# Kernel tuning notes

Hardware: AMD Instinct MI355X
Metric: run time of the kernel (lower is better)

Reference implementation:

```python
import jax, jax.numpy as jnp
import numpy as np

L, H, D, A, T = 2, 8, 512, 64, 256  # layers, heads, model_dim, attention_dim, target_dim
B, S = 2, 2048
EPS = 1e-5


def _ln(x, g, b):
    m = jnp.mean(x, axis=-1, keepdims=True)
    v = jnp.mean((x - m) ** 2, axis=-1, keepdims=True)
    return (x - m) / jnp.sqrt(v + EPS) * g + b


def setup_inputs() -> dict:
    key = jax.random.key(0)
    ks = jax.random.split(key, 16)
    s = 0.02
    inp = {
        "x": jax.random.normal(ks[0], (B, S, D), jnp.float32),
        # per-head QKV projections, stacked over layers and heads
        "Wq": jax.random.normal(ks[1], (L, H, D, A), jnp.float32) * s,
        "bq": jnp.zeros((L, H, A), jnp.float32),
        "Wk": jax.random.normal(ks[2], (L, H, D, A), jnp.float32) * s,
        "bk": jnp.zeros((L, H, A), jnp.float32),
        "Wv": jax.random.normal(ks[3], (L, H, D, A), jnp.float32) * s,
        "bv": jnp.zeros((L, H, A), jnp.float32),
        # output projection of concatenated heads: [H*A, D]
        "Wo": jax.random.normal(ks[4], (L, H * A, D), jnp.float32) * s,
        "bo": jnp.zeros((L, D), jnp.float32),
        # AddNorm after attention
        "ln1_g": jnp.ones((L, D), jnp.float32),
        "ln1_b": jnp.zeros((L, D), jnp.float32),
        # FFN (hidden_dim == model_dim in this module)
        "W1": jax.random.normal(ks[5], (L, D, D), jnp.float32) * s,
        "b1": jnp.zeros((L, D), jnp.float32),
        "W2": jax.random.normal(ks[6], (L, D, D), jnp.float32) * s,
        "b2": jnp.zeros((L, D), jnp.float32),
        # AddNorm after FFN
        "ln2_g": jnp.ones((L, D), jnp.float32),
        "ln2_b": jnp.zeros((L, D), jnp.float32),
        # final projection to target_dim
        "Wp": jax.random.normal(ks[7], (D, T), jnp.float32) * s,
        "bp": jnp.zeros((T,), jnp.float32),
    }
    return inp


def reference(x, Wq, bq, Wk, bk, Wv, bv, Wo, bo, ln1_g, ln1_b,
              W1, b1, W2, b2, ln2_g, ln2_b, Wp, bp):
    scale = 1.0 / jnp.sqrt(jnp.asarray(A, x.dtype))
    for i in range(L):
        # batched per-head QKV projections (math identical to per-head Linears)
        q = jnp.einsum('bsd,hda->bhsa', x, Wq[i]) + bq[i][:, None, :]
        k = jnp.einsum('bsd,hda->bhsa', x, Wk[i]) + bk[i][:, None, :]
        v = jnp.einsum('bsd,hda->bhsa', x, Wv[i]) + bv[i][:, None, :]
        scores = jnp.einsum('bhsa,bhta->bhst', q, k) * scale  # [B,H,S,S]
        attn = jax.nn.softmax(scores, axis=-1)
        heads = jnp.einsum('bhst,bhta->bhsa', attn, v)        # [B,H,S,A]
        concat = heads.transpose(0, 2, 1, 3).reshape(x.shape[0], x.shape[1], H * A)
        mha = concat @ Wo[i] + bo[i]
        x = _ln(x + mha, ln1_g[i], ln1_b[i])
        ffn = jax.nn.relu(x @ W1[i] + b1[i]) @ W2[i] + b2[i]
        x = _ln(x + ffn, ln2_g[i], ln2_b[i])
    return x @ Wp + bp
```

## Files before the change

kernel.cpp:

```cpp
#include <hip/hip_runtime.h>
#include <hip/hip_bf16.h>

#define MDIM 4096
#define DDIM 512
#define ADIM 64
#define HHEADS 8
#define SLEN 2048
#define TDIM 256

typedef __attribute__((ext_vector_type(8))) short short8;
typedef __attribute__((ext_vector_type(16))) float f32x16;

__device__ __forceinline__ unsigned short f2bf(float f) {
    union { __hip_bfloat16 h; unsigned short u; } c;
    c.h = __float2bfloat16(f);
    return c.u;
}
__device__ __forceinline__ float bf2f(short s) {
    return __uint_as_float((unsigned)(unsigned short)s << 16);
}

#define N1 524288
#define N2 524288
#define NP 131072
__global__ __launch_bounds__(256) void prep_k(
    const float* __restrict__ Wq, const float* __restrict__ Wk, const float* __restrict__ Wv,
    const float* __restrict__ Wo, const float* __restrict__ W1, const float* __restrict__ W2,
    const float* __restrict__ Wp, const float* __restrict__ x,
    short* __restrict__ Wqt, short* __restrict__ Wkt, short* __restrict__ Wvt,
    short* __restrict__ Wot, short* __restrict__ W1t, short* __restrict__ W2t,
    short* __restrict__ Wpt, short* __restrict__ xbf)
{
    long idx = (long)blockIdx.x * 256 + threadIdx.x;
    if (idx < 3L * N1) {
        int t = (int)(idx / N1);
        int r = (int)(idx % N1);
        int a = r & 63, k = (r >> 6) & 511, hh = r >> 15;
        const float* src = (t == 0) ? Wq : (t == 1) ? Wk : Wv;
        short* dst = (t == 0) ? Wqt : (t == 1) ? Wkt : Wvt;
        dst[((size_t)hh << 15) + (a << 9) + k] = (short)f2bf(src[r]);
        return;
    }
    idx -= 3L * N1;
    if (idx < 3L * N2) {
        int t = (int)(idx / N2);
        int r = (int)(idx % N2);
        int n = r & 511, k = (r >> 9) & 511, i = r >> 18;
        const float* src = (t == 0) ? Wo : (t == 1) ? W1 : W2;
        short* dst = (t == 0) ? Wot : (t == 1) ? W1t : W2t;
        dst[((size_t)i << 18) + (n << 9) + k] = (short)f2bf(src[r]);
        return;
    }
    idx -= 3L * N2;
    if (idx < NP) {
        int r = (int)idx;
        int n = r & 255, k = r >> 8;
        Wpt[n * 512 + k] = (short)f2bf(Wp[r]);
        return;
    }
    idx -= NP;
    xbf[idx] = (short)f2bf(x[idx]);
}

#define LDT 66
__global__ __launch_bounds__(256, 2) void gemm_bf(
    const short* __restrict__ A, const short* __restrict__ Bt,
    const float* __restrict__ bias, void* __restrict__ Cout,
    int M, int N, int K, int flags)
{
    __shared__ short As[64 * LDT];
    __shared__ short Bs[64 * LDT];
    const int tid = threadIdx.x;
    const int wave = tid >> 6, lane = tid & 63;
    const int l31 = lane & 31, hi = lane >> 5;
    const int wm = wave >> 1, wn = wave & 1;
    const int m0 = blockIdx.y * 64, n0 = blockIdx.x * 64;

    f32x16 acc;
#pragma unroll
    for (int r = 0; r < 16; ++r) acc[r] = 0.f;

    const int sr = tid >> 2;
    const int sc = (tid & 3) * 16;

    for (int k0 = 0; k0 < K; k0 += 64) {
        __syncthreads();
        *(short8*)&As[sr * LDT + sc]     = *(const short8*)&A[(size_t)(m0 + sr) * K + k0 + sc];
        *(short8*)&As[sr * LDT + sc + 8] = *(const short8*)&A[(size_t)(m0 + sr) * K + k0 + sc + 8];
        *(short8*)&Bs[sr * LDT + sc]     = *(const short8*)&Bt[(size_t)(n0 + sr) * K + k0 + sc];
        *(short8*)&Bs[sr * LDT + sc + 8] = *(const short8*)&Bt[(size_t)(n0 + sr) * K + k0 + sc + 8];
        __syncthreads();

        short8 af[4], bfm[4];
#pragma unroll
        for (int ks = 0; ks < 4; ++ks) {
            af[ks]  = *(const short8*)&As[(wm * 32 + l31) * LDT + ks * 16 + hi * 8];
            bfm[ks] = *(const short8*)&Bs[(wn * 32 + l31) * LDT + ks * 16 + hi * 8];
        }
#pragma unroll
        for (int ks = 0; ks < 4; ++ks)
            acc = __builtin_amdgcn_mfma_f32_32x32x16_bf16(af[ks], bfm[ks], acc, 0, 0, 0);
    }

    const int col = n0 + wn * 32 + l31;
    const float bb = bias[col];
    const int rbase = m0 + wm * 32 + 4 * hi;
#pragma unroll
    for (int r = 0; r < 16; ++r) {
        int row = rbase + (r & 3) + 8 * (r >> 2);
        float v = acc[r] + bb;
        if (flags & 1) v = fmaxf(v, 0.f);
        if (flags & 2) ((short*)Cout)[(size_t)row * N + col] = (short)f2bf(v);
        else           ((float*)Cout)[(size_t)row * N + col] = v;
    }
}

#define EXPC 0.1803368801111244f

__global__ __launch_bounds__(256, 2) void qkv_bf(
    const short* __restrict__ A,
    const short* __restrict__ Wqt, const short* __restrict__ Wkt, const short* __restrict__ Wvt,
    const float* __restrict__ bq, const float* __restrict__ bk, const float* __restrict__ bv,
    short* __restrict__ Oq, short* __restrict__ Ok, short* __restrict__ Ov)
{
    __shared__ short As[128 * LDT];
    __shared__ short Bs[64 * LDT];
    const int tid = threadIdx.x;
    const int wave = tid >> 6, lane = tid & 63;
    const int l31 = lane & 31, hi = lane >> 5;
    const int wm = wave >> 1, wn = wave & 1;
    const int m0 = blockIdx.y * 128;
    const int nt = blockIdx.x;
    const int which = nt >> 3, h = nt & 7;

    const short* Bt = ((which == 0) ? Wqt : (which == 1) ? Wkt : Wvt) + (size_t)h * 64 * 512;
    const float* bias = ((which == 0) ? bq : (which == 1) ? bk : bv) + h * 64;
    short* Out = (which == 0) ? Oq : (which == 1) ? Ok : Ov;

    f32x16 acc[2];
#pragma unroll
    for (int ms = 0; ms < 2; ++ms)
#pragma unroll
        for (int r = 0; r < 16; ++r) acc[ms][r] = 0.f;

    const int sr = tid >> 3;
    const int sc = (tid & 7) * 8;

    for (int k0 = 0; k0 < 512; k0 += 64) {
        __syncthreads();
#pragma unroll
        for (int p = 0; p < 4; ++p)
            *(short8*)&As[(p * 32 + sr) * LDT + sc] =
                *(const short8*)&A[(size_t)(m0 + p * 32 + sr) * 512 + k0 + sc];
#pragma unroll
        for (int p = 0; p < 2; ++p)
            *(short8*)&Bs[(p * 32 + sr) * LDT + sc] =
                *(const short8*)&Bt[(size_t)(p * 32 + sr) * 512 + k0 + sc];
        __syncthreads();

        short8 af[2][4], bfm[4];
#pragma unroll
        for (int ms = 0; ms < 2; ++ms)
#pragma unroll
            for (int ks = 0; ks < 4; ++ks)
                af[ms][ks] = *(const short8*)&As[(wm * 64 + ms * 32 + l31) * LDT + ks * 16 + hi * 8];
#pragma unroll
        for (int ks = 0; ks < 4; ++ks)
            bfm[ks] = *(const short8*)&Bs[(wn * 32 + l31) * LDT + ks * 16 + hi * 8];
#pragma unroll
        for (int ms = 0; ms < 2; ++ms)
#pragma unroll
            for (int ks = 0; ks < 4; ++ks)
                acc[ms] = __builtin_amdgcn_mfma_f32_32x32x16_bf16(af[ms][ks], bfm[ks], acc[ms], 0, 0, 0);
    }

    const int a = wn * 32 + l31;
    const float bb = bias[a];
    const int b = m0 >> 11;
    const int sb = (m0 & (SLEN - 1)) + wm * 64;
    const int bh = b * HHEADS + h;

    if (which == 0) {
        short* Ob = Out + (size_t)bh * SLEN * 64;
#pragma unroll
        for (int ms = 0; ms < 2; ++ms)
#pragma unroll
            for (int r = 0; r < 16; ++r) {
                int s = sb + ms * 32 + (r & 3) + 8 * (r >> 2) + 4 * hi;
                Ob[(size_t)s * 64 + a] = (short)f2bf((acc[ms][r] + bb) * EXPC);
            }
    } else if (which == 1) {
        short* Ob = Out + (size_t)bh * SLEN * 64;
#pragma unroll
        for (int ms = 0; ms < 2; ++ms)
#pragma unroll
            for (int r = 0; r < 16; ++r) {
                int s = sb + ms * 32 + (r & 3) + 8 * (r >> 2) + 4 * hi;
                Ob[(size_t)s * 64 + a] = (short)f2bf(acc[ms][r] + bb);
            }
    } else {
        short* Ob = Out + ((size_t)bh * 64 + a) * SLEN;
#pragma unroll
        for (int ms = 0; ms < 2; ++ms)
#pragma unroll
            for (int g = 0; g < 4; ++g) {
                int s = sb + ms * 32 + 8 * g + 4 * hi;
                ushort4 w;
                w.x = f2bf(acc[ms][4 * g + 0] + bb);
                w.y = f2bf(acc[ms][4 * g + 1] + bb);
                w.z = f2bf(acc[ms][4 * g + 2] + bb);
                w.w = f2bf(acc[ms][4 * g + 3] + bb);
                *(ushort4*)&Ob[s] = w;
            }
    }
}

__global__ __launch_bounds__(256, 2) void attn_mfma(
    const short* __restrict__ Qb, const short* __restrict__ Kb,
    const short* __restrict__ Vtb, short* __restrict__ hc)
{
    __shared__ float Ols[4][64][66];
    __shared__ float Lls[4][64];

    const int tid = threadIdx.x;
    const int wid = tid >> 6;
    const int lane = tid & 63;
    const int l31 = lane & 31;
    const int hi = lane >> 5;

    const int wg = blockIdx.x;
    const int swz = (wg & 7) * 64 + (wg >> 3);
    const int qt = swz & 31;
    const int bh = swz >> 5;

    const short* Qg = Qb + (size_t)bh * SLEN * 64;
    const short* Kg = Kb + (size_t)bh * SLEN * 64;
    const short* Vg = Vtb + (size_t)bh * 64 * SLEN;

    const int q0 = qt * 64;

    short8 qf[2][4];
#pragma unroll
    for (int nt = 0; nt < 2; ++nt)
#pragma unroll
        for (int ks = 0; ks < 4; ++ks)
            qf[nt][ks] = *(const short8*)&Qg[(size_t)(q0 + nt * 32 + l31) * 64 + ks * 16 + hi * 8];

    f32x16 oacc[2][2];
    float lsum[2] = {0.f, 0.f};
#pragma unroll
    for (int nt = 0; nt < 2; ++nt)
#pragma unroll
        for (int dt = 0; dt < 2; ++dt)
#pragma unroll
            for (int r = 0; r < 16; ++r) oacc[nt][dt][r] = 0.f;

    const int kw = wid * (SLEN / 4);

#pragma unroll 1
    for (int kt = 0; kt < 8; ++kt) {
        const int k0 = kw + kt * 64;

        short8 kf[2][4], vf[2][4];
#pragma unroll
        for (int mt = 0; mt < 2; ++mt)
#pragma unroll
            for (int ks = 0; ks < 4; ++ks)
                kf[mt][ks] = *(const short8*)&Kg[(size_t)(k0 + mt * 32 + l31) * 64 + ks * 16 + hi * 8];
#pragma unroll
        for (int dt = 0; dt < 2; ++dt)
#pragma unroll
            for (int p = 0; p < 4; ++p)
                vf[dt][p] = *(const short8*)&Vg[(size_t)(dt * 32 + l31) * SLEN + k0 + p * 16 + hi * 8];

#pragma unroll
        for (int nt = 0; nt < 2; ++nt) {
            f32x16 sacc[2];
            __builtin_amdgcn_s_setprio(1);
#pragma unroll
            for (int mt = 0; mt < 2; ++mt) {
                f32x16 s;
#pragma unroll
                for (int r = 0; r < 16; ++r) s[r] = 0.f;
#pragma unroll
                for (int ks = 0; ks < 4; ++ks)
                    s = __builtin_amdgcn_mfma_f32_32x32x16_bf16(kf[mt][ks], qf[nt][ks], s, 0, 0, 0);
                sacc[mt] = s;
            }
            __builtin_amdgcn_s_setprio(0);

            int2 pk[2][4];
#pragma unroll
            for (int mt = 0; mt < 2; ++mt)
#pragma unroll
                for (int g = 0; g < 4; ++g) {
                    unsigned a0 = __float_as_uint(__builtin_amdgcn_exp2f(sacc[mt][4 * g + 0]));
                    unsigned a1 = __float_as_uint(__builtin_amdgcn_exp2f(sacc[mt][4 * g + 1]));
                    unsigned a2 = __float_as_uint(__builtin_amdgcn_exp2f(sacc[mt][4 * g + 2]));
                    unsigned a3 = __float_as_uint(__builtin_amdgcn_exp2f(sacc[mt][4 * g + 3]));
                    float t0 = __uint_as_float(a0 & 0xffff0000u);
                    float t1 = __uint_as_float(a1 & 0xffff0000u);
                    float t2 = __uint_as_float(a2 & 0xffff0000u);
                    float t3 = __uint_as_float(a3 & 0xffff0000u);
                    lsum[nt] += (t0 + t1) + (t2 + t3);
                    pk[mt][g].x = (int)__builtin_amdgcn_perm(a1, a0, 0x07060302u);
                    pk[mt][g].y = (int)__builtin_amdgcn_perm(a3, a2, 0x07060302u);
                }

            int2 xch[2][2];
#pragma unroll
            for (int mt = 0; mt < 2; ++mt)
#pragma unroll
                for (int h2 = 0; h2 < 2; ++h2) {
                    int2 v = hi ? pk[mt][2 * h2] : pk[mt][2 * h2 + 1];
                    xch[mt][h2].x = __shfl_xor(v.x, 32);
                    xch[mt][h2].y = __shfl_xor(v.y, 32);
                }

            __builtin_amdgcn_s_setprio(1);
#pragma unroll
            for (int p = 0; p < 4; ++p) {
                const int mt = p >> 1, h2 = p & 1;
                const int ga = 2 * h2, gb = 2 * h2 + 1;
                const int2 X = xch[mt][h2];
                union { int4 i; short8 s; } u;
                u.i.x = hi ? X.x : pk[mt][ga].x;
                u.i.y = hi ? X.y : pk[mt][ga].y;
                u.i.z = hi ? pk[mt][gb].x : X.x;
                u.i.w = hi ? pk[mt][gb].y : X.y;
#pragma unroll
                for (int dt = 0; dt < 2; ++dt)
                    oacc[nt][dt] = __builtin_amdgcn_mfma_f32_32x32x16_bf16(u.s, vf[dt][p], oacc[nt][dt], 0, 0, 0);
            }
            __builtin_amdgcn_s_setprio(0);
        }
    }

#pragma unroll
    for (int nt = 0; nt < 2; ++nt) {
        float lt = lsum[nt] + __shfl_xor(lsum[nt], 32);
        if (hi == 0) Lls[wid][nt * 32 + l31] = lt;
#pragma unroll
        for (int dt = 0; dt < 2; ++dt)
#pragma unroll
            for (int r = 0; r < 16; ++r) {
                int q = nt * 32 + (r & 3) + 8 * (r >> 2) + 4 * hi;
                Ols[wid][q][dt * 32 + l31] = oacc[nt][dt][r];
            }
    }
    __syncthreads();

    const int b = bh >> 3, h = bh & 7;
    const int q = tid >> 2;
    const int c0 = (tid & 3) * 16;
    const float inv = 1.f / (Lls[0][q] + Lls[1][q] + Lls[2][q] + Lls[3][q]);
    short* orow = hc + ((size_t)(b * SLEN + q0 + q)) * DDIM + h * 64 + c0;
#pragma unroll
    for (int half = 0; half < 2; ++half) {
        short8 o8;
#pragma unroll
        for (int j = 0; j < 8; ++j) {
            int d = c0 + half * 8 + j;
            o8[j] = (short)f2bf((Ols[0][q][d] + Ols[1][q][d] + Ols[2][q][d] + Ols[3][q][d]) * inv);
        }
        *(short8*)&orow[half * 8] = o8;
    }
}

__global__ __launch_bounds__(256) void addnorm_bf(
    short* __restrict__ X, const float* __restrict__ Y,
    const float* __restrict__ g, const float* __restrict__ beta)
{
    const int lane = threadIdx.x & 63;
    const int t = blockIdx.x * 4 + (threadIdx.x >> 6);
    short* xr = X + (size_t)t * DDIM;
    const float* yr = Y + (size_t)t * DDIM;
    const int c0 = lane * 8;

    short8 x8 = *(const short8*)&xr[c0];
    float4 y0 = *(const float4*)&yr[c0];
    float4 y1 = *(const float4*)&yr[c0 + 4];
    float v[8];
    v[0] = bf2f(x8[0]) + y0.x; v[1] = bf2f(x8[1]) + y0.y;
    v[2] = bf2f(x8[2]) + y0.z; v[3] = bf2f(x8[3]) + y0.w;
    v[4] = bf2f(x8[4]) + y1.x; v[5] = bf2f(x8[5]) + y1.y;
    v[6] = bf2f(x8[6]) + y1.z; v[7] = bf2f(x8[7]) + y1.w;

    float s1 = 0.f, s2 = 0.f;
#pragma unroll
    for (int j = 0; j < 8; ++j) { s1 += v[j]; s2 += v[j] * v[j]; }
#pragma unroll
    for (int off = 1; off < 64; off <<= 1) {
        s1 += __shfl_xor(s1, off);
        s2 += __shfl_xor(s2, off);
    }
    float mean = s1 * (1.0f / DDIM);
    float var = s2 * (1.0f / DDIM) - mean * mean;
    float rstd = rsqrtf(var + 1e-5f);

    float4 ga = *(const float4*)&g[c0];
    float4 gb = *(const float4*)&g[c0 + 4];
    float4 ba = *(const float4*)&beta[c0];
    float4 bb = *(const float4*)&beta[c0 + 4];
    float gg[8] = {ga.x, ga.y, ga.z, ga.w, gb.x, gb.y, gb.z, gb.w};
    float bt[8] = {ba.x, ba.y, ba.z, ba.w, bb.x, bb.y, bb.z, bb.w};

    short8 o8;
#pragma unroll
    for (int j = 0; j < 8; ++j)
        o8[j] = (short)f2bf((v[j] - mean) * rstd * gg[j] + bt[j]);
    *(short8*)&xr[c0] = o8;
}

extern "C" void kernel_launch(void* const* d_in, const int* in_sizes, int n_in,
                              void* d_out, int out_size, void* d_ws, size_t ws_size,
                              hipStream_t stream)
{
    (void)in_sizes; (void)n_in; (void)out_size; (void)ws_size;
    const float* x   = (const float*)d_in[0];
    const float* Wq  = (const float*)d_in[1];
    const float* bq  = (const float*)d_in[2];
    const float* Wk  = (const float*)d_in[3];
    const float* bk  = (const float*)d_in[4];
    const float* Wv  = (const float*)d_in[5];
    const float* bv  = (const float*)d_in[6];
    const float* Wo  = (const float*)d_in[7];
    const float* bo  = (const float*)d_in[8];
    const float* g1  = (const float*)d_in[9];
    const float* be1 = (const float*)d_in[10];
    const float* W1  = (const float*)d_in[11];
    const float* b1  = (const float*)d_in[12];
    const float* W2  = (const float*)d_in[13];
    const float* b2  = (const float*)d_in[14];
    const float* g2  = (const float*)d_in[15];
    const float* be2 = (const float*)d_in[16];
    const float* Wp  = (const float*)d_in[17];
    const float* bp  = (const float*)d_in[18];

    char* wsb = (char*)d_ws;
    const size_t MB = 1024 * 1024;
    short* xbf   = (short*)(wsb + 0);
    short* Qbuf  = (short*)(wsb + 4 * MB);
    short* Kbuf  = (short*)(wsb + 8 * MB);
    short* Vtbuf = (short*)(wsb + 12 * MB);
    short* hcbf  = (short*)(wsb + 16 * MB);
    float* y     = (float*)(wsb + 20 * MB);
    short* hidbf = (short*)(wsb + 28 * MB);
    short* Wqt   = (short*)(wsb + 33 * MB);
    short* Wkt   = (short*)(wsb + 34 * MB);
    short* Wvt   = (short*)(wsb + 35 * MB);
    short* Wot   = (short*)(wsb + 36 * MB);
    short* W1t   = (short*)(wsb + 37 * MB);
    short* W2t   = (short*)(wsb + 38 * MB);
    short* Wpt   = (short*)(wsb + 39 * MB);

    prep_k<<<20992, 256, 0, stream>>>(Wq, Wk, Wv, Wo, W1, W2, Wp, x,
                                      Wqt, Wkt, Wvt, Wot, W1t, W2t, Wpt, xbf);

    for (int i = 0; i < 2; ++i) {
        const size_t wOffQ = (size_t)i * 262144;
        const size_t wOffS = (size_t)i * 262144;
        qkv_bf<<<dim3(24, 32), 256, 0, stream>>>(
            xbf, Wqt + wOffQ, Wkt + wOffQ, Wvt + wOffQ,
            bq + i * 512, bk + i * 512, bv + i * 512,
            Qbuf, Kbuf, Vtbuf);
        attn_mfma<<<512, 256, 0, stream>>>(Qbuf, Kbuf, Vtbuf, hcbf);
        gemm_bf<<<dim3(8, 64), 256, 0, stream>>>(
            hcbf, Wot + wOffS, bo + i * 512, y, MDIM, DDIM, DDIM, 0);
        addnorm_bf<<<1024, 256, 0, stream>>>(xbf, y, g1 + i * 512, be1 + i * 512);
        gemm_bf<<<dim3(8, 64), 256, 0, stream>>>(
            xbf, W1t + wOffS, b1 + i * 512, hidbf, MDIM, DDIM, DDIM, 3);
        gemm_bf<<<dim3(8, 64), 256, 0, stream>>>(
            hidbf, W2t + wOffS, b2 + i * 512, y, MDIM, DDIM, DDIM, 0);
        addnorm_bf<<<1024, 256, 0, stream>>>(xbf, y, g2 + i * 512, be2 + i * 512);
    }
    gemm_bf<<<dim3(4, 64), 256, 0, stream>>>(
        xbf, Wpt, bp, (float*)d_out, MDIM, TDIM, DDIM, 0);
}
```

Before: 304.2 us.

## Restructure attention, enlarge GEMM tiles, and tile weight-transpose prep through LDS

```diff
diff --git a/kernel.cpp b/kernel.cpp
--- a/kernel.cpp
+++ b/kernel.cpp
@@ -3,10 +3,11 @@
 
 #define MDIM 4096
 #define DDIM 512
-#define ADIM 64
 #define HHEADS 8
 #define SLEN 2048
 #define TDIM 256
+#define LDT 66
+#define EXPC 0.1803368801111244f
 
 typedef __attribute__((ext_vector_type(8))) short short8;
 typedef __attribute__((ext_vector_type(16))) float f32x16;
@@ -20,9 +21,6 @@
     return __uint_as_float((unsigned)(unsigned short)s << 16);
 }
 
-#define N1 524288
-#define N2 524288
-#define NP 131072
 __global__ __launch_bounds__(256) void prep_k(
     const float* __restrict__ Wq, const float* __restrict__ Wk, const float* __restrict__ Wv,
     const float* __restrict__ Wo, const float* __restrict__ W1, const float* __restrict__ W2,
@@ -31,91 +29,132 @@
     short* __restrict__ Wot, short* __restrict__ W1t, short* __restrict__ W2t,
     short* __restrict__ Wpt, short* __restrict__ xbf)
 {
-    long idx = (long)blockIdx.x * 256 + threadIdx.x;
-    if (idx < 3L * N1) {
-        int t = (int)(idx / N1);
-        int r = (int)(idx % N1);
-        int a = r & 63, k = (r >> 6) & 511, hh = r >> 15;
-        const float* src = (t == 0) ? Wq : (t == 1) ? Wk : Wv;
-        short* dst = (t == 0) ? Wqt : (t == 1) ? Wkt : Wvt;
-        dst[((size_t)hh << 15) + (a << 9) + k] = (short)f2bf(src[r]);
+    __shared__ short T[64][72];
+    const int b = blockIdx.x, tid = threadIdx.x;
+
+    if (b >= 800) {
+        const int idx = (b - 800) * 256 + tid;
+        for (int e = idx; e < 262144; e += 65536) {
+            float4 f0 = *(const float4*)&x[e * 8];
+            float4 f1 = *(const float4*)&x[e * 8 + 4];
+            short8 o;
+            o[0] = (short)f2bf(f0.x); o[1] = (short)f2bf(f0.y);
+            o[2] = (short)f2bf(f0.z); o[3] = (short)f2bf(f0.w);
+            o[4] = (short)f2bf(f1.x); o[5] = (short)f2bf(f1.y);
+            o[6] = (short)f2bf(f1.z); o[7] = (short)f2bf(f1.w);
+            *(short8*)&xbf[e * 8] = o;
+        }
         return;
     }
-    idx -= 3L * N1;
-    if (idx < 3L * N2) {
-        int t = (int)(idx / N2);
-        int r = (int)(idx % N2);
-        int n = r & 511, k = (r >> 9) & 511, i = r >> 18;
-        const float* src = (t == 0) ? Wo : (t == 1) ? W1 : W2;
-        short* dst = (t == 0) ? Wot : (t == 1) ? W1t : W2t;
-        dst[((size_t)i << 18) + (n << 9) + k] = (short)f2bf(src[r]);
-        return;
-    }
-    idx -= 3L * N2;
-    if (idx < NP) {
-        int r = (int)idx;
-        int n = r & 255, k = r >> 8;
-        Wpt[n * 512 + k] = (short)f2bf(Wp[r]);
-        return;
-    }
-    idx -= NP;
-    xbf[idx] = (short)f2bf(x[idx]);
-}
-
-#define LDT 66
+
+    const float* srcp; short* dstp; int ss;
+    if (b < 384) {
+        int w = b >> 7, t = b & 127;
+        int lh = t >> 3, kt0 = (t & 7) << 6;
+        const float* W = (w == 0) ? Wq : (w == 1) ? Wk : Wv;
+        short* Wt = (w == 0) ? Wqt : (w == 1) ? Wkt : Wvt;
+        srcp = W + (size_t)lh * 32768 + (size_t)kt0 * 64;
+        dstp = Wt + (size_t)lh * 32768 + kt0;
+        ss = 64;
+    } else if (b < 768) {
+        int w = (b - 384) >> 7, t = (b - 384) & 127;
+        int l = t >> 6, tt = t & 63;
+        int kt0 = (tt >> 3) << 6, nt0 = (tt & 7) << 6;
+        const float* W = (w == 0) ? Wo : (w == 1) ? W1 : W2;
+        short* Wt = (w == 0) ? Wot : (w == 1) ? W1t : W2t;
+        srcp = W + (size_t)l * 262144 + (size_t)kt0 * 512 + nt0;
+        dstp = Wt + (size_t)l * 262144 + (size_t)nt0 * 512 + kt0;
+        ss = 512;
+    } else {
+        int t = b - 768;
+        int kt0 = (t >> 2) << 6, nt0 = (t & 3) << 6;
+        srcp = Wp + (size_t)kt0 * 256 + nt0;
+        dstp = Wpt + (size_t)nt0 * 512 + kt0;
+        ss = 256;
+    }
+
+    const int r = tid >> 2, c0 = (tid & 3) * 16;
+#pragma unroll
+    for (int j = 0; j < 16; j += 4) {
+        float4 f = *(const float4*)&srcp[(size_t)r * ss + c0 + j];
+        T[r][c0 + j + 0] = (short)f2bf(f.x);
+        T[r][c0 + j + 1] = (short)f2bf(f.y);
+        T[r][c0 + j + 2] = (short)f2bf(f.z);
+        T[r][c0 + j + 3] = (short)f2bf(f.w);
+    }
+    __syncthreads();
+    short8 o0, o1;
+#pragma unroll
+    for (int j = 0; j < 8; ++j) { o0[j] = T[c0 + j][r]; o1[j] = T[c0 + 8 + j][r]; }
+    *(short8*)&dstp[(size_t)r * 512 + c0] = o0;
+    *(short8*)&dstp[(size_t)r * 512 + c0 + 8] = o1;
+}
+
 __global__ __launch_bounds__(256, 2) void gemm_bf(
     const short* __restrict__ A, const short* __restrict__ Bt,
     const float* __restrict__ bias, void* __restrict__ Cout,
-    int M, int N, int K, int flags)
+    int N, int K, int flags)
 {
-    __shared__ short As[64 * LDT];
+    __shared__ short As[128 * LDT];
     __shared__ short Bs[64 * LDT];
     const int tid = threadIdx.x;
     const int wave = tid >> 6, lane = tid & 63;
     const int l31 = lane & 31, hi = lane >> 5;
     const int wm = wave >> 1, wn = wave & 1;
-    const int m0 = blockIdx.y * 64, n0 = blockIdx.x * 64;
-
-    f32x16 acc;
-#pragma unroll
-    for (int r = 0; r < 16; ++r) acc[r] = 0.f;
-
-    const int sr = tid >> 2;
-    const int sc = (tid & 3) * 16;
+    const int m0 = blockIdx.y * 128, n0 = blockIdx.x * 64;
+
+    f32x16 acc[2];
+#pragma unroll
+    for (int ms = 0; ms < 2; ++ms)
+#pragma unroll
+        for (int r = 0; r < 16; ++r) acc[ms][r] = 0.f;
+
+    const int sr = tid >> 3;
+    const int sc = (tid & 7) * 8;
 
     for (int k0 = 0; k0 < K; k0 += 64) {
         __syncthreads();
-        *(short8*)&As[sr * LDT + sc]     = *(const short8*)&A[(size_t)(m0 + sr) * K + k0 + sc];
-        *(short8*)&As[sr * LDT + sc + 8] = *(const short8*)&A[(size_t)(m0 + sr) * K + k0 + sc + 8];
-        *(short8*)&Bs[sr * LDT + sc]     = *(const short8*)&Bt[(size_t)(n0 + sr) * K + k0 + sc];
-        *(short8*)&Bs[sr * LDT + sc + 8] = *(const short8*)&Bt[(size_t)(n0 + sr) * K + k0 + sc + 8];
+#pragma unroll
+        for (int p = 0; p < 4; ++p)
+            *(short8*)&As[(p * 32 + sr) * LDT + sc] =
+                *(const short8*)&A[(size_t)(m0 + p * 32 + sr) * K + k0 + sc];
+#pragma unroll
+        for (int p = 0; p < 2; ++p)
+            *(short8*)&Bs[(p * 32 + sr) * LDT + sc] =
+                *(const short8*)&Bt[(size_t)(n0 + p * 32 + sr) * K + k0 + sc];
         __syncthreads();
 
-        short8 af[4], bfm[4];
-#pragma unroll
-        for (int ks = 0; ks < 4; ++ks) {
-            af[ks]  = *(const short8*)&As[(wm * 32 + l31) * LDT + ks * 16 + hi * 8];
+        short8 af[2][4], bfm[4];
+#pragma unroll
+        for (int ms = 0; ms < 2; ++ms)
+#pragma unroll
+            for (int ks = 0; ks < 4; ++ks)
+                af[ms][ks] = *(const short8*)&As[(wm * 64 + ms * 32 + l31) * LDT + ks * 16 + hi * 8];
+#pragma unroll
+        for (int ks = 0; ks < 4; ++ks)
             bfm[ks] = *(const short8*)&Bs[(wn * 32 + l31) * LDT + ks * 16 + hi * 8];
-        }
-#pragma unroll
-        for (int ks = 0; ks < 4; ++ks)
-            acc = __builtin_amdgcn_mfma_f32_32x32x16_bf16(af[ks], bfm[ks], acc, 0, 0, 0);
+#pragma unroll
+        for (int ms = 0; ms < 2; ++ms)
+#pragma unroll
+            for (int ks = 0; ks < 4; ++ks)
+                acc[ms] = __builtin_amdgcn_mfma_f32_32x32x16_bf16(af[ms][ks], bfm[ks], acc[ms], 0, 0, 0);
     }
 
     const int col = n0 + wn * 32 + l31;
     const float bb = bias[col];
-    const int rbase = m0 + wm * 32 + 4 * hi;
-#pragma unroll
-    for (int r = 0; r < 16; ++r) {
-        int row = rbase + (r & 3) + 8 * (r >> 2);
-        float v = acc[r] + bb;
-        if (flags & 1) v = fmaxf(v, 0.f);
-        if (flags & 2) ((short*)Cout)[(size_t)row * N + col] = (short)f2bf(v);
-        else           ((float*)Cout)[(size_t)row * N + col] = v;
-    }
-}
-
-#define EXPC 0.1803368801111244f
+#pragma unroll
+    for (int ms = 0; ms < 2; ++ms) {
+        const int rbase = m0 + wm * 64 + ms * 32 + 4 * hi;
+#pragma unroll
+        for (int r = 0; r < 16; ++r) {
+            int row = rbase + (r & 3) + 8 * (r >> 2);
+            float v = acc[ms][r] + bb;
+            if (flags & 1) v = fmaxf(v, 0.f);
+            if (flags & 2) ((short*)Cout)[(size_t)row * N + col] = (short)f2bf(v);
+            else           ((float*)Cout)[(size_t)row * N + col] = v;
+        }
+    }
+}
 
 __global__ __launch_bounds__(256, 2) void qkv_bf(
     const short* __restrict__ A,
@@ -219,8 +258,8 @@
     const short* __restrict__ Qb, const short* __restrict__ Kb,
     const short* __restrict__ Vtb, short* __restrict__ hc)
 {
-    __shared__ float Ols[4][64][66];
-    __shared__ float Lls[4][64];
+    __shared__ short Ks[64 * 72];
+    __shared__ short Vs[64 * 72];
 
     const int tid = threadIdx.x;
     const int wid = tid >> 6;
@@ -228,142 +267,136 @@
     const int l31 = lane & 31;
     const int hi = lane >> 5;
 
-    const int wg = blockIdx.x;
-    const int swz = (wg & 7) * 64 + (wg >> 3);
-    const int qt = swz & 31;
-    const int bh = swz >> 5;
+    const int bidx = blockIdx.x;
+    const int swz = (bidx & 7) * 32 + (bidx >> 3);
+    const int qt = swz & 15, bh = swz >> 4;
 
     const short* Qg = Qb + (size_t)bh * SLEN * 64;
     const short* Kg = Kb + (size_t)bh * SLEN * 64;
     const short* Vg = Vtb + (size_t)bh * 64 * SLEN;
 
-    const int q0 = qt * 64;
-
-    short8 qf[2][4];
-#pragma unroll
-    for (int nt = 0; nt < 2; ++nt)
-#pragma unroll
-        for (int ks = 0; ks < 4; ++ks)
-            qf[nt][ks] = *(const short8*)&Qg[(size_t)(q0 + nt * 32 + l31) * 64 + ks * 16 + hi * 8];
-
-    f32x16 oacc[2][2];
-    float lsum[2] = {0.f, 0.f};
-#pragma unroll
-    for (int nt = 0; nt < 2; ++nt)
+    const int q0 = qt * 128 + wid * 32;
+
+    short8 qf[4];
+#pragma unroll
+    for (int ks = 0; ks < 4; ++ks)
+        qf[ks] = *(const short8*)&Qg[(size_t)(q0 + l31) * 64 + ks * 16 + hi * 8];
+
+    f32x16 oacc[2];
+    float lsum = 0.f;
+#pragma unroll
+    for (int dt = 0; dt < 2; ++dt)
+#pragma unroll
+        for (int r = 0; r < 16; ++r) oacc[dt][r] = 0.f;
+
+    const int srow = tid >> 2;
+    const int sch = (tid & 3) * 16;
+
+    short8 rk0 = *(const short8*)&Kg[(size_t)srow * 64 + sch];
+    short8 rk1 = *(const short8*)&Kg[(size_t)srow * 64 + sch + 8];
+    short8 rv0 = *(const short8*)&Vg[(size_t)srow * SLEN + sch];
+    short8 rv1 = *(const short8*)&Vg[(size_t)srow * SLEN + sch + 8];
+
+#pragma unroll 1
+    for (int kt = 0; kt < 32; ++kt) {
+        __syncthreads();
+        *(short8*)&Ks[srow * 72 + sch]     = rk0;
+        *(short8*)&Ks[srow * 72 + sch + 8] = rk1;
+        *(short8*)&Vs[srow * 72 + sch]     = rv0;
+        *(short8*)&Vs[srow * 72 + sch + 8] = rv1;
+        __syncthreads();
+
+        if (kt < 31) {
+            const int k0n = (kt + 1) * 64;
+            rk0 = *(const short8*)&Kg[(size_t)(k0n + srow) * 64 + sch];
+            rk1 = *(const short8*)&Kg[(size_t)(k0n + srow) * 64 + sch + 8];
+            rv0 = *(const short8*)&Vg[(size_t)srow * SLEN + k0n + sch];
+            rv1 = *(const short8*)&Vg[(size_t)srow * SLEN + k0n + sch + 8];
+        }
+
+        short8 kf[2][4], vf[2][4];
+#pragma unroll
+        for (int mt = 0; mt < 2; ++mt)
+#pragma unroll
+            for (int ks = 0; ks < 4; ++ks)
+                kf[mt][ks] = *(const short8*)&Ks[(mt * 32 + l31) * 72 + ks * 16 + hi * 8];
 #pragma unroll
         for (int dt = 0; dt < 2; ++dt)
 #pragma unroll
-            for (int r = 0; r < 16; ++r) oacc[nt][dt][r] = 0.f;
-
-    const int kw = wid * (SLEN / 4);
-
-#pragma unroll 1
-    for (int kt = 0; kt < 8; ++kt) {
-        const int k0 = kw + kt * 64;
-
-        short8 kf[2][4], vf[2][4];
+            for (int p = 0; p < 4; ++p)
+                vf[dt][p] = *(const short8*)&Vs[(dt * 32 + l31) * 72 + p * 16 + hi * 8];
+
+        f32x16 sacc[2];
+        __builtin_amdgcn_s_setprio(1);
+#pragma unroll
+        for (int mt = 0; mt < 2; ++mt) {
+            f32x16 s;
+#pragma unroll
+            for (int r = 0; r < 16; ++r) s[r] = 0.f;
+#pragma unroll
+            for (int ks = 0; ks < 4; ++ks)
+                s = __builtin_amdgcn_mfma_f32_32x32x16_bf16(kf[mt][ks], qf[ks], s, 0, 0, 0);
+            sacc[mt] = s;
+        }
+        __builtin_amdgcn_s_setprio(0);
+
+        int2 pk[2][4];
 #pragma unroll
         for (int mt = 0; mt < 2; ++mt)
 #pragma unroll
-            for (int ks = 0; ks < 4; ++ks)
-                kf[mt][ks] = *(const short8*)&Kg[(size_t)(k0 + mt * 32 + l31) * 64 + ks * 16 + hi * 8];
+            for (int g = 0; g < 4; ++g) {
+                unsigned a0 = __float_as_uint(__builtin_amdgcn_exp2f(sacc[mt][4 * g + 0]));
+                unsigned a1 = __float_as_uint(__builtin_amdgcn_exp2f(sacc[mt][4 * g + 1]));
+                unsigned a2 = __float_as_uint(__builtin_amdgcn_exp2f(sacc[mt][4 * g + 2]));
+                unsigned a3 = __float_as_uint(__builtin_amdgcn_exp2f(sacc[mt][4 * g + 3]));
+                float t0 = __uint_as_float(a0 & 0xffff0000u);
+                float t1 = __uint_as_float(a1 & 0xffff0000u);
+                float t2 = __uint_as_float(a2 & 0xffff0000u);
+                float t3 = __uint_as_float(a3 & 0xffff0000u);
+                lsum += (t0 + t1) + (t2 + t3);
+                pk[mt][g].x = (int)__builtin_amdgcn_perm(a1, a0, 0x07060302u);
+                pk[mt][g].y = (int)__builtin_amdgcn_perm(a3, a2, 0x07060302u);
+            }
+
+        int2 xch[2][2];
+#pragma unroll
+        for (int mt = 0; mt < 2; ++mt)
+#pragma unroll
+            for (int h2 = 0; h2 < 2; ++h2) {
+                int2 v = hi ? pk[mt][2 * h2] : pk[mt][2 * h2 + 1];
+                xch[mt][h2].x = __shfl_xor(v.x, 32);
+                xch[mt][h2].y = __shfl_xor(v.y, 32);
+            }
+
+        __builtin_amdgcn_s_setprio(1);
+#pragma unroll
+        for (int p = 0; p < 4; ++p) {
+            const int mt = p >> 1, h2 = p & 1;
+            const int ga = 2 * h2, gb = 2 * h2 + 1;
+            const int2 X = xch[mt][h2];
+            union { int4 i; short8 s; } u;
+            u.i.x = hi ? X.x : pk[mt][ga].x;
+            u.i.y = hi ? X.y : pk[mt][ga].y;
+            u.i.z = hi ? pk[mt][gb].x : X.x;
+            u.i.w = hi ? pk[mt][gb].y : X.y;
+#pragma unroll
+            for (int dt = 0; dt < 2; ++dt)
+                oacc[dt] = __builtin_amdgcn_mfma_f32_32x32x16_bf16(u.s, vf[dt][p], oacc[dt], 0, 0, 0);
+        }
+        __builtin_amdgcn_s_setprio(0);
+    }
+
+    const float lt = lsum + __shfl_xor(lsum, 32);
+    const float invl = 1.f / lt;
+    const int b = bh >> 3, h = bh & 7;
+#pragma unroll
+    for (int r = 0; r < 16; ++r) {
+        const int qrow = (r & 3) + 8 * (r >> 2) + 4 * hi;
+        const float iv = __shfl(invl, qrow);
+        const size_t rowb = ((size_t)(b * SLEN + q0 + qrow)) * DDIM + h * 64;
 #pragma unroll
         for (int dt = 0; dt < 2; ++dt)
-#pragma unroll
-            for (int p = 0; p < 4; ++p)
-                vf[dt][p] = *(const short8*)&Vg[(size_t)(dt * 32 + l31) * SLEN + k0 + p * 16 + hi * 8];
-
-#pragma unroll
-        for (int nt = 0; nt < 2; ++nt) {
-            f32x16 sacc[2];
-            __builtin_amdgcn_s_setprio(1);
-#pragma unroll
-            for (int mt = 0; mt < 2; ++mt) {
-                f32x16 s;
-#pragma unroll
-                for (int r = 0; r < 16; ++r) s[r] = 0.f;
-#pragma unroll
-                for (int ks = 0; ks < 4; ++ks)
-                    s = __builtin_amdgcn_mfma_f32_32x32x16_bf16(kf[mt][ks], qf[nt][ks], s, 0, 0, 0);
-                sacc[mt] = s;
-            }
-            __builtin_amdgcn_s_setprio(0);
-
-            int2 pk[2][4];
-#pragma unroll
-            for (int mt = 0; mt < 2; ++mt)
-#pragma unroll
-                for (int g = 0; g < 4; ++g) {
-                    unsigned a0 = __float_as_uint(__builtin_amdgcn_exp2f(sacc[mt][4 * g + 0]));
-                    unsigned a1 = __float_as_uint(__builtin_amdgcn_exp2f(sacc[mt][4 * g + 1]));
-                    unsigned a2 = __float_as_uint(__builtin_amdgcn_exp2f(sacc[mt][4 * g + 2]));
-                    unsigned a3 = __float_as_uint(__builtin_amdgcn_exp2f(sacc[mt][4 * g + 3]));
-                    float t0 = __uint_as_float(a0 & 0xffff0000u);
-                    float t1 = __uint_as_float(a1 & 0xffff0000u);
-                    float t2 = __uint_as_float(a2 & 0xffff0000u);
-                    float t3 = __uint_as_float(a3 & 0xffff0000u);
-                    lsum[nt] += (t0 + t1) + (t2 + t3);
-                    pk[mt][g].x = (int)__builtin_amdgcn_perm(a1, a0, 0x07060302u);
-                    pk[mt][g].y = (int)__builtin_amdgcn_perm(a3, a2, 0x07060302u);
-                }
-
-            int2 xch[2][2];
-#pragma unroll
-            for (int mt = 0; mt < 2; ++mt)
-#pragma unroll
-                for (int h2 = 0; h2 < 2; ++h2) {
-                    int2 v = hi ? pk[mt][2 * h2] : pk[mt][2 * h2 + 1];
-                    xch[mt][h2].x = __shfl_xor(v.x, 32);
-                    xch[mt][h2].y = __shfl_xor(v.y, 32);
-                }
-
-            __builtin_amdgcn_s_setprio(1);
-#pragma unroll
-            for (int p = 0; p < 4; ++p) {
-                const int mt = p >> 1, h2 = p & 1;
-                const int ga = 2 * h2, gb = 2 * h2 + 1;
-                const int2 X = xch[mt][h2];
-                union { int4 i; short8 s; } u;
-                u.i.x = hi ? X.x : pk[mt][ga].x;
-                u.i.y = hi ? X.y : pk[mt][ga].y;
-                u.i.z = hi ? pk[mt][gb].x : X.x;
-                u.i.w = hi ? pk[mt][gb].y : X.y;
-#pragma unroll
-                for (int dt = 0; dt < 2; ++dt)
-                    oacc[nt][dt] = __builtin_amdgcn_mfma_f32_32x32x16_bf16(u.s, vf[dt][p], oacc[nt][dt], 0, 0, 0);
-            }
-            __builtin_amdgcn_s_setprio(0);
-        }
-    }
-
-#pragma unroll
-    for (int nt = 0; nt < 2; ++nt) {
-        float lt = lsum[nt] + __shfl_xor(lsum[nt], 32);
-        if (hi == 0) Lls[wid][nt * 32 + l31] = lt;
-#pragma unroll
-        for (int dt = 0; dt < 2; ++dt)
-#pragma unroll
-            for (int r = 0; r < 16; ++r) {
-                int q = nt * 32 + (r & 3) + 8 * (r >> 2) + 4 * hi;
-                Ols[wid][q][dt * 32 + l31] = oacc[nt][dt][r];
-            }
-    }
-    __syncthreads();
-
-    const int b = bh >> 3, h = bh & 7;
-    const int q = tid >> 2;
-    const int c0 = (tid & 3) * 16;
-    const float inv = 1.f / (Lls[0][q] + Lls[1][q] + Lls[2][q] + Lls[3][q]);
-    short* orow = hc + ((size_t)(b * SLEN + q0 + q)) * DDIM + h * 64 + c0;
-#pragma unroll
-    for (int half = 0; half < 2; ++half) {
-        short8 o8;
-#pragma unroll
-        for (int j = 0; j < 8; ++j) {
-            int d = c0 + half * 8 + j;
-            o8[j] = (short)f2bf((Ols[0][q][d] + Ols[1][q][d] + Ols[2][q][d] + Ols[3][q][d]) * inv);
-        }
-        *(short8*)&orow[half * 8] = o8;
+            hc[rowb + dt * 32 + l31] = (short)f2bf(oacc[dt][r] * iv);
     }
 }
 
@@ -454,26 +487,25 @@
     short* W2t   = (short*)(wsb + 38 * MB);
     short* Wpt   = (short*)(wsb + 39 * MB);
 
-    prep_k<<<20992, 256, 0, stream>>>(Wq, Wk, Wv, Wo, W1, W2, Wp, x,
-                                      Wqt, Wkt, Wvt, Wot, W1t, W2t, Wpt, xbf);
+    prep_k<<<1056, 256, 0, stream>>>(Wq, Wk, Wv, Wo, W1, W2, Wp, x,
+                                     Wqt, Wkt, Wvt, Wot, W1t, W2t, Wpt, xbf);
 
     for (int i = 0; i < 2; ++i) {
-        const size_t wOffQ = (size_t)i * 262144;
-        const size_t wOffS = (size_t)i * 262144;
+        const size_t wOff = (size_t)i * 262144;
         qkv_bf<<<dim3(24, 32), 256, 0, stream>>>(
-            xbf, Wqt + wOffQ, Wkt + wOffQ, Wvt + wOffQ,
+            xbf, Wqt + wOff, Wkt + wOff, Wvt + wOff,
             bq + i * 512, bk + i * 512, bv + i * 512,
             Qbuf, Kbuf, Vtbuf);
-        attn_mfma<<<512, 256, 0, stream>>>(Qbuf, Kbuf, Vtbuf, hcbf);
-        gemm_bf<<<dim3(8, 64), 256, 0, stream>>>(
-            hcbf, Wot + wOffS, bo + i * 512, y, MDIM, DDIM, DDIM, 0);
+        attn_mfma<<<256, 256, 0, stream>>>(Qbuf, Kbuf, Vtbuf, hcbf);
+        gemm_bf<<<dim3(8, 32), 256, 0, stream>>>(
+            hcbf, Wot + wOff, bo + i * 512, y, 512, 512, 0);
         addnorm_bf<<<1024, 256, 0, stream>>>(xbf, y, g1 + i * 512, be1 + i * 512);
-        gemm_bf<<<dim3(8, 64), 256, 0, stream>>>(
-            xbf, W1t + wOffS, b1 + i * 512, hidbf, MDIM, DDIM, DDIM, 3);
-        gemm_bf<<<dim3(8, 64), 256, 0, stream>>>(
-            hidbf, W2t + wOffS, b2 + i * 512, y, MDIM, DDIM, DDIM, 0);
+        gemm_bf<<<dim3(8, 32), 256, 0, stream>>>(
+            xbf, W1t + wOff, b1 + i * 512, hidbf, 512, 512, 3);
+        gemm_bf<<<dim3(8, 32), 256, 0, stream>>>(
+            hidbf, W2t + wOff, b2 + i * 512, y, 512, 512, 0);
         addnorm_bf<<<1024, 256, 0, stream>>>(xbf, y, g2 + i * 512, be2 + i * 512);
     }
-    gemm_bf<<<dim3(4, 64), 256, 0, stream>>>(
-        xbf, Wpt, bp, (float*)d_out, MDIM, TDIM, DDIM, 0);
-}
+    gemm_bf<<<dim3(4, 32), 256, 0, stream>>>(
+        xbf, Wpt, bp, (float*)d_out, 256, 512, 0);
+}
```

After: 370.6 us. 1.22x slower.
